# Optimization experiments

Measured on AMD Instinct MI355X. Metric: run time of the kernel, lower is better.

The kernel has to match this reference:

```python
import jax, jax.numpy as jnp
import numpy as np

# Module config (mirrors init_kwargs)
B = 131072          # batch of trajectories
N_STATES = 16       # n_x_f + n_x_b
N_SEL = 8           # states selected per subnet (band width of Binary_mat)
N_U = 4             # inputs
N_FEAT = 64         # hidden width, neuron_list = [64, 64]
N_OUT = 16          # n_x_o, one output per subnet

# Binary_mat[i, j] = 1 iff (j - i) mod 16 < 8. The torch loop collects selected
# indices in INCREASING j order, so sort each row's selected set.
IDX = np.sort((np.arange(N_OUT)[:, None] + np.arange(N_SEL)[None, :]) % N_STATES, axis=1)  # [16, 8] int


def setup_inputs() -> dict:
    key = jax.random.key(0)
    k0, k1, k2, k3, k4, k5 = jax.random.split(key, 6)
    zin = N_SEL + N_U  # 12 = per-subnet MLP input width
    return {
        "x_f": jax.random.normal(k0, (B, 8), jnp.float32),
        "x_b": jax.random.normal(k1, (B, 8), jnp.float32),
        "u": jax.random.normal(k2, (B, N_U), jnp.float32),
        # stacked per-subnet weights (nn.Linear stores [out, in]); no biases
        "W0": jax.random.normal(k3, (N_OUT, N_FEAT, zin), jnp.float32) * 0.05,
        "W1": jax.random.normal(k4, (N_OUT, N_FEAT, N_FEAT), jnp.float32) * 0.05,
        "W2": jax.random.normal(k5, (N_OUT, 1, N_FEAT), jnp.float32) * 0.05,
    }


def reference(x_f, x_b, u, W0, W1, W2):
    # x_tilde = cat(x_f, x_b): [B, 16]
    x_tilde = jnp.concatenate([x_f, x_b], axis=-1)
    # Per-subnet gather of its selected state subset: [B, 16(sub), 8]
    x_sel = x_tilde[:, IDX]
    # Append exogenous input u to every subnet's input: [B, 16, 12]
    u_b = jnp.broadcast_to(u[:, None, :], (u.shape[0], N_OUT, N_U))
    z = jnp.concatenate([x_sel, u_b], axis=-1)
    # Grouped small MLPs (Linear+Tanh, Linear+Tanh, Linear) as batched GEMMs
    h = jnp.tanh(jnp.einsum('bsi,soi->bso', z, W0))   # [B, 16, 64]
    h = jnp.tanh(jnp.einsum('bsh,soh->bso', h, W1))   # [B, 16, 64]
    dx = jnp.einsum('bsh,soh->bso', h, W2)[..., 0]    # scatter into dx slices -> [B, 16]
    return dx
```

## Files before the change

kernel.cpp:

```cpp
#include <hip/hip_runtime.h>


#define N_STATES 16
#define CHUNK    4
#define TANH_SCALE 2.885390081777927f

typedef _Float16 f16x8 __attribute__((ext_vector_type(8)));
typedef float    f32x4 __attribute__((ext_vector_type(4)));

__device__ __forceinline__ unsigned int pack_f16(float a, float b) {
    auto p = __builtin_amdgcn_cvt_pkrtz(a, b);
    union { decltype(p) h; unsigned int u; } cv{p};
    return cv.u;
}

__device__ __forceinline__ float sig_r(float ps) {
    float e = __builtin_amdgcn_exp2f(ps);
    return __builtin_amdgcn_rcpf(e + 1.0f);
}
__device__ __forceinline__ float tanh_from_scaled(float ps) {
    return __builtin_fmaf(-2.0f, sig_r(ps), 1.0f);
}

__global__ __launch_bounds__(256, 4) void fans_mfma_kernel(
    const float* __restrict__ x_f, const float* __restrict__ x_b,
    const float* __restrict__ u,   const float* __restrict__ W0,
    const float* __restrict__ W1,  const float* __restrict__ W2,
    float* __restrict__ out)
{
    __shared__ __align__(16) uint4 zpl[2 * 256];
    __shared__ __align__(16) unsigned int Hd[4][16][36];

    const int s   = blockIdx.y;
    const int tid = threadIdx.x;
    const int b0  = blockIdx.x * (256 * CHUNK);

    const int lid = tid & 63;
    const int w   = tid >> 6;
    const int c   = lid & 15;
    const int q   = lid >> 4;

    f16x8 a0[4];
    {
        const float* w0s = W0 + s * 768;
        #pragma unroll
        for (int t = 0; t < 4; ++t) {
            #pragma unroll
            for (int j = 0; j < 8; ++j) {
                const int k = 8 * q + j;
                const float v = (k < 12) ? w0s[(16 * t + c) * 12 + k] * TANH_SCALE : 0.0f;
                a0[t][j] = (_Float16)v;
            }
        }
    }
    f16x8 a1[2][4];
    {
        const float* w1s = W1 + s * 4096;
        #pragma unroll
        for (int ks = 0; ks < 2; ++ks) {
            #pragma unroll
            for (int t = 0; t < 4; ++t) {
                const float4* p = (const float4*)(w1s + (16 * t + c) * 64 + 32 * ks + 8 * q);
                const float4 v0 = p[0], v1 = p[1];
                a1[ks][t] = (f16x8){(_Float16)(v0.x * TANH_SCALE), (_Float16)(v0.y * TANH_SCALE),
                                    (_Float16)(v0.z * TANH_SCALE), (_Float16)(v0.w * TANH_SCALE),
                                    (_Float16)(v1.x * TANH_SCALE), (_Float16)(v1.y * TANH_SCALE),
                                    (_Float16)(v1.z * TANH_SCALE), (_Float16)(v1.w * TANH_SCALE)};
            }
        }
    }
    float w2n[16];
    float sumw2 = 0.0f;
    {
        const float* w2s = W2 + s * 64;
        #pragma unroll
        for (int t = 0; t < 4; ++t)
            #pragma unroll
            for (int r = 0; r < 4; ++r) {
                const float v = w2s[16 * t + 4 * q + r];
                w2n[4 * t + r] = -2.0f * v;
                sumw2 += v;
            }
    }

    const int wrap = (s > 8) ? (s - 8) : 0;

    #pragma unroll 1
    for (int ch = 0; ch < CHUNK; ++ch) {
        const int rbase = b0 + ch * 256;

        {
            const int row = rbase + tid;
            float zs[8];
            #pragma unroll
            for (int j = 0; j < 8; ++j) {
                const int idx = (j < wrap) ? j : (s + j - wrap);
                zs[j] = (idx < 8) ? x_f[row * 8 + idx] : x_b[row * 8 + (idx - 8)];
            }
            const float4 uv = *(const float4*)(u + row * 4);
            zpl[tid] = make_uint4(pack_f16(zs[0], zs[1]), pack_f16(zs[2], zs[3]),
                                  pack_f16(zs[4], zs[5]), pack_f16(zs[6], zs[7]));
            zpl[256 + tid] = make_uint4(pack_f16(uv.x, uv.y), pack_f16(uv.z, uv.w), 0u, 0u);
        }

        #pragma unroll
        for (int m = 0; m < 4; ++m) {
            const int rowb = 64 * w + 16 * m;

            f16x8 zf = {0, 0, 0, 0, 0, 0, 0, 0};
            if (q < 2) {
                const uint4 zv = zpl[q * 256 + rowb + c];
                union { uint4 v; f16x8 h; } cz{zv};
                zf = cz.h;
            }

            f32x4 c1[4];
            #pragma unroll
            for (int t = 0; t < 4; ++t)
                c1[t] = __builtin_amdgcn_mfma_f32_16x16x32_f16(
                    a0[t], zf, (f32x4){0.f, 0.f, 0.f, 0.f}, 0, 0, 0);

            #pragma unroll
            for (int t = 0; t < 4; ++t) {
                *(uint2*)&Hd[w][c][8 * t + 2 * q] =
                    make_uint2(pack_f16(tanh_from_scaled(c1[t][0]), tanh_from_scaled(c1[t][1])),
                               pack_f16(tanh_from_scaled(c1[t][2]), tanh_from_scaled(c1[t][3])));
            }

            f32x4 c2[4] = {{0.f, 0.f, 0.f, 0.f}, {0.f, 0.f, 0.f, 0.f},
                           {0.f, 0.f, 0.f, 0.f}, {0.f, 0.f, 0.f, 0.f}};
            #pragma unroll
            for (int ks = 0; ks < 2; ++ks) {
                const uint4 hv = *(const uint4*)&Hd[w][c][16 * ks + 4 * q];
                union { uint4 v; f16x8 h; } bb{hv};
                #pragma unroll
                for (int t = 0; t < 4; ++t)
                    c2[t] = __builtin_amdgcn_mfma_f32_16x16x32_f16(a1[ks][t], bb.h, c2[t], 0, 0, 0);
            }

            float acc = sumw2;
            #pragma unroll
            for (int t = 0; t < 4; ++t)
                #pragma unroll
                for (int r = 0; r < 4; ++r)
                    acc = __builtin_fmaf(sig_r(c2[t][r]), w2n[4 * t + r], acc);
            acc += __shfl_xor(acc, 16);
            acc += __shfl_xor(acc, 32);

            if (lid < 16)
                out[(rbase + rowb + lid) * N_STATES + s] = acc;
        }
    }
}

extern "C" void kernel_launch(void* const* d_in, const int* in_sizes, int n_in,
                              void* d_out, int out_size, void* d_ws, size_t ws_size,
                              hipStream_t stream) {
    const float* x_f = (const float*)d_in[0];
    const float* x_b = (const float*)d_in[1];
    const float* u   = (const float*)d_in[2];
    const float* W0  = (const float*)d_in[3];
    const float* W1  = (const float*)d_in[4];
    const float* W2  = (const float*)d_in[5];
    float* out = (float*)d_out;

    const int nb = in_sizes[0] / 8;
    dim3 grid(nb / (256 * CHUNK), N_STATES);
    fans_mfma_kernel<<<grid, 256, 0, stream>>>(x_f, x_b, u, W0, W1, W2, out);
}
```

Before: 146.5 us.

## Stage per-subnet fp16 weights in LDS to cut registers and raise occupancy

Weight fragments for W0 and W1 are no longer held in VGPRs for the whole kernel. The first wave converts them to fp16 and writes them to shared memory, and every wave reloads them from LDS before each MFMA. Launch bounds go from 4 to 5 waves per SIMD, and the u staging buffer shrinks to uint2. This trades register pressure for extra LDS traffic and a block-wide barrier. It also removes the redundant global weight loads that every wave made before.

```diff
diff --git a/kernel.cpp b/kernel.cpp
--- a/kernel.cpp
+++ b/kernel.cpp
@@ -13,6 +13,12 @@
     union { decltype(p) h; unsigned int u; } cv{p};
     return cv.u;
 }
+__device__ __forceinline__ f16x8 u4_to_h8(uint4 v) {
+    union { uint4 u; f16x8 h; } x; x.u = v; return x.h;
+}
+__device__ __forceinline__ uint4 h8_to_u4(f16x8 h) {
+    union { f16x8 h; uint4 u; } x; x.h = h; return x.u;
+}
 
 __device__ __forceinline__ float sig_r(float ps) {
     float e = __builtin_amdgcn_exp2f(ps);
@@ -22,14 +28,17 @@
     return __builtin_fmaf(-2.0f, sig_r(ps), 1.0f);
 }
 
-__global__ __launch_bounds__(256, 4) void fans_mfma_kernel(
+__global__ __launch_bounds__(256, 5) void fans_mfma_kernel(
     const float* __restrict__ x_f, const float* __restrict__ x_b,
     const float* __restrict__ u,   const float* __restrict__ W0,
     const float* __restrict__ W1,  const float* __restrict__ W2,
     float* __restrict__ out)
 {
-    __shared__ __align__(16) uint4 zpl[2 * 256];
+    __shared__ __align__(16) uint4 zplA[256];
+    __shared__ __align__(16) uint2 zplB[256];
     __shared__ __align__(16) unsigned int Hd[4][16][36];
+    __shared__ __align__(16) uint4 sA0[4][32];
+    __shared__ __align__(16) uint4 sA1[8][64];
 
     const int s   = blockIdx.y;
     const int tid = threadIdx.x;
@@ -40,21 +49,20 @@
     const int c   = lid & 15;
     const int q   = lid >> 4;
 
-    f16x8 a0[4];
-    {
-        const float* w0s = W0 + s * 768;
-        #pragma unroll
-        for (int t = 0; t < 4; ++t) {
+    if (tid < 64) {
+        if (q < 2) {
+            const float* w0s = W0 + s * 768;
             #pragma unroll
-            for (int j = 0; j < 8; ++j) {
-                const int k = 8 * q + j;
-                const float v = (k < 12) ? w0s[(16 * t + c) * 12 + k] * TANH_SCALE : 0.0f;
-                a0[t][j] = (_Float16)v;
+            for (int t = 0; t < 4; ++t) {
+                f16x8 v;
+                #pragma unroll
+                for (int j = 0; j < 8; ++j) {
+                    const int k = 8 * q + j;
+                    v[j] = (_Float16)((k < 12) ? w0s[(16 * t + c) * 12 + k] * TANH_SCALE : 0.0f);
+                }
+                sA0[t][lid] = h8_to_u4(v);
             }
         }
-    }
-    f16x8 a1[2][4];
-    {
         const float* w1s = W1 + s * 4096;
         #pragma unroll
         for (int ks = 0; ks < 2; ++ks) {
@@ -62,13 +70,15 @@
             for (int t = 0; t < 4; ++t) {
                 const float4* p = (const float4*)(w1s + (16 * t + c) * 64 + 32 * ks + 8 * q);
                 const float4 v0 = p[0], v1 = p[1];
-                a1[ks][t] = (f16x8){(_Float16)(v0.x * TANH_SCALE), (_Float16)(v0.y * TANH_SCALE),
-                                    (_Float16)(v0.z * TANH_SCALE), (_Float16)(v0.w * TANH_SCALE),
-                                    (_Float16)(v1.x * TANH_SCALE), (_Float16)(v1.y * TANH_SCALE),
-                                    (_Float16)(v1.z * TANH_SCALE), (_Float16)(v1.w * TANH_SCALE)};
+                f16x8 v = {(_Float16)(v0.x * TANH_SCALE), (_Float16)(v0.y * TANH_SCALE),
+                           (_Float16)(v0.z * TANH_SCALE), (_Float16)(v0.w * TANH_SCALE),
+                           (_Float16)(v1.x * TANH_SCALE), (_Float16)(v1.y * TANH_SCALE),
+                           (_Float16)(v1.z * TANH_SCALE), (_Float16)(v1.w * TANH_SCALE)};
+                sA1[ks * 4 + t][lid] = h8_to_u4(v);
             }
         }
     }
+
     float w2n[16];
     float sumw2 = 0.0f;
     {
@@ -82,6 +92,8 @@
                 sumw2 += v;
             }
     }
+
+    __syncthreads();
 
     const int wrap = (s > 8) ? (s - 8) : 0;
 
@@ -98,9 +110,9 @@
                 zs[j] = (idx < 8) ? x_f[row * 8 + idx] : x_b[row * 8 + (idx - 8)];
             }
             const float4 uv = *(const float4*)(u + row * 4);
-            zpl[tid] = make_uint4(pack_f16(zs[0], zs[1]), pack_f16(zs[2], zs[3]),
-                                  pack_f16(zs[4], zs[5]), pack_f16(zs[6], zs[7]));
-            zpl[256 + tid] = make_uint4(pack_f16(uv.x, uv.y), pack_f16(uv.z, uv.w), 0u, 0u);
+            zplA[tid] = make_uint4(pack_f16(zs[0], zs[1]), pack_f16(zs[2], zs[3]),
+                                   pack_f16(zs[4], zs[5]), pack_f16(zs[6], zs[7]));
+            zplB[tid] = make_uint2(pack_f16(uv.x, uv.y), pack_f16(uv.z, uv.w));
         }
 
         #pragma unroll
@@ -108,17 +120,21 @@
             const int rowb = 64 * w + 16 * m;
 
             f16x8 zf = {0, 0, 0, 0, 0, 0, 0, 0};
-            if (q < 2) {
-                const uint4 zv = zpl[q * 256 + rowb + c];
-                union { uint4 v; f16x8 h; } cz{zv};
-                zf = cz.h;
+            if (q == 0) {
+                zf = u4_to_h8(zplA[rowb + c]);
+            } else if (q == 1) {
+                const uint2 b = zplB[rowb + c];
+                zf = u4_to_h8(make_uint4(b.x, b.y, 0u, 0u));
             }
 
             f32x4 c1[4];
             #pragma unroll
-            for (int t = 0; t < 4; ++t)
+            for (int t = 0; t < 4; ++t) {
+                f16x8 a0t = {0, 0, 0, 0, 0, 0, 0, 0};
+                if (q < 2) a0t = u4_to_h8(sA0[t][lid]);
                 c1[t] = __builtin_amdgcn_mfma_f32_16x16x32_f16(
-                    a0[t], zf, (f32x4){0.f, 0.f, 0.f, 0.f}, 0, 0, 0);
+                    a0t, zf, (f32x4){0.f, 0.f, 0.f, 0.f}, 0, 0, 0);
+            }
 
             #pragma unroll
             for (int t = 0; t < 4; ++t) {
@@ -131,11 +147,12 @@
                            {0.f, 0.f, 0.f, 0.f}, {0.f, 0.f, 0.f, 0.f}};
             #pragma unroll
             for (int ks = 0; ks < 2; ++ks) {
-                const uint4 hv = *(const uint4*)&Hd[w][c][16 * ks + 4 * q];
-                union { uint4 v; f16x8 h; } bb{hv};
+                const f16x8 hb = u4_to_h8(*(const uint4*)&Hd[w][c][16 * ks + 4 * q]);
                 #pragma unroll
-                for (int t = 0; t < 4; ++t)
-                    c2[t] = __builtin_amdgcn_mfma_f32_16x16x32_f16(a1[ks][t], bb.h, c2[t], 0, 0, 0);
+                for (int t = 0; t < 4; ++t) {
+                    const f16x8 a1t = u4_to_h8(sA1[ks * 4 + t][lid]);
+                    c2[t] = __builtin_amdgcn_mfma_f32_16x16x32_f16(a1t, hb, c2[t], 0, 0, 0);
+                }
             }
 
             float acc = sumw2;
```

New measurement: 138.0 us. 1.06x faster.
